# Performance work log

Measured on AMD Instinct MI355X. Metric: run time of the kernel, lower is better.

The kernel has to match this reference:

```python
import jax, jax.numpy as jnp
import numpy as np

N_WL = 296      # spectral points after dropping last 4
POOL = 4
FM = N_WL // POOL  # 74
HEAD = 64
EMB = 48


def setup_inputs() -> dict:
    key = jax.random.key(0)
    ks = jax.random.split(key, 16)
    B = 2048
    inp = {
        "x": jax.random.uniform(ks[0], (B, 300), dtype=jnp.float32),
        # FeaturePicker DI
        "wDI": jax.random.normal(ks[1], (HEAD, FM, FM), dtype=jnp.float32),
        "bDI": jax.random.normal(ks[2], (HEAD,), dtype=jnp.float32),
        "fcDI_w": jax.random.normal(ks[3], (EMB, HEAD), dtype=jnp.float32) * 0.1,
        "fcDI_b": jax.random.normal(ks[4], (EMB,), dtype=jnp.float32) * 0.1,
        # FeaturePicker NDI
        "wNDI": jax.random.normal(ks[5], (HEAD, FM, FM), dtype=jnp.float32),
        "bNDI": jax.random.normal(ks[6], (HEAD,), dtype=jnp.float32),
        "fcNDI_w": jax.random.normal(ks[7], (EMB, HEAD), dtype=jnp.float32) * 0.1,
        "fcNDI_b": jax.random.normal(ks[8], (EMB,), dtype=jnp.float32) * 0.1,
        # head MLP
        "fc1_w": jax.random.normal(ks[9], (48, 96), dtype=jnp.float32) * 0.1,
        "fc1_b": jax.random.normal(ks[10], (48,), dtype=jnp.float32) * 0.1,
        "l1_w": jax.random.normal(ks[11], (20, 48), dtype=jnp.float32) * 0.1,
        "l1_b": jax.random.normal(ks[12], (20,), dtype=jnp.float32) * 0.1,
        "l2_w": jax.random.normal(ks[13], (1, 20), dtype=jnp.float32) * 0.1,
        "l2_b": jax.random.normal(ks[14], (1,), dtype=jnp.float32) * 0.1,
    }
    return inp


def _feature_picker(m, wmap, bias, fw, fb):
    # m: [B, 296, 296] -> avgpool 4x4 -> [B, 74, 74]
    B = m.shape[0]
    p = m.reshape(B, FM, POOL, FM, POOL).mean(axis=(2, 4))
    # weighted sum against each of HEAD weight maps (== [B,5476] @ [5476,HEAD])
    h = jnp.einsum('bij,hij->bh', p, wmap) + bias
    h = jax.nn.elu(h)
    return jax.nn.elu(h @ fw.T + fb)  # [B, EMB]


def reference(x, wDI, bDI, fcDI_w, fcDI_b, wNDI, bNDI, fcNDI_w, fcNDI_b,
              fc1_w, fc1_b, l1_w, l1_b, l2_w, l2_b):
    x0 = x[:, :-4]                       # [B, 296]
    a = x0[:, None, :]                   # unsqueeze(1)
    b = x0[:, :, None]                   # unsqueeze(2)
    DI = a - b                           # [B, 296, 296]
    NDI = (a - b) / (a + b + 1e-5)
    eDI = _feature_picker(DI, wDI, bDI, fcDI_w, fcDI_b)
    eNDI = _feature_picker(NDI, wNDI, bNDI, fcNDI_w, fcNDI_b)
    emb = jnp.concatenate([eDI, eNDI], axis=1)      # [B, 96]
    emb = jax.nn.elu(emb @ fc1_w.T + fc1_b)
    emb = jax.nn.elu(emb @ l1_w.T + l1_b)
    return jax.nn.sigmoid(emb @ l2_w.T + l2_b)      # [B, 1]
```

## Files before the change

### kernel.cpp

```cpp
#include <hip/hip_runtime.h>
#include <hip/hip_bf16.h>
#include <math.h>

#define NWL    296
#define FMD    74
#define HEAD   64
#define EMBD   48
#define BATCH  2048
#define XCOLS  300
#define NPAIR  2701
#define NPAIR_P 3072
#define KCH    768
#define MR     8

#define WS_CMR  0
#define WS_PAIR (FMD * HEAD)
#define WS_WATT (WS_PAIR + NPAIR_P)

typedef _Float16 f16x8 __attribute__((ext_vector_type(8)));
typedef float f32x4 __attribute__((ext_vector_type(4)));

__device__ __forceinline__ float eluf(float x) { return x > 0.f ? x : expm1f(x); }

__device__ __forceinline__ void pair_decode(int k, int& I, int& J) {
  I = (int)((147.0f - sqrtf(21609.0f - 8.0f * (float)k)) * 0.5f);
  int base = (I * (147 - I)) >> 1;
  while (base > k) { I--; base = (I * (147 - I)) >> 1; }
  while (I < 72 && ((I + 1) * (146 - I)) / 2 <= k) { I++; base = (I * (147 - I)) >> 1; }
  J = I + 1 + (k - base);
}

__global__ __launch_bounds__(256) void fcr_prep_v5(
    const float* __restrict__ wDI,
    const float* __restrict__ wNDI,
    float* __restrict__ ws) {
  __shared__ float wdL[FMD * FMD];
  __shared__ float wnL[FMD * FMD];

  int t = threadIdx.x;
  int h = blockIdx.x;

  const float4* gd = (const float4*)(wDI + (size_t)h * FMD * FMD);
  const float4* gn = (const float4*)(wNDI + (size_t)h * FMD * FMD);
  for (int i = t; i < FMD * FMD / 4; i += 256) {
    ((float4*)wdL)[i] = gd[i];
    ((float4*)wnL)[i] = gn[i];
  }
  __syncthreads();

  _Float16* wATt = (_Float16*)(ws + WS_WATT);
  for (int k = t; k < NPAIR_P; k += 256) {
    float v = 0.f;
    if (k < NPAIR) {
      int I, J; pair_decode(k, I, J);
      v = (wnL[I * FMD + J] - wnL[J * FMD + I]) * 0.0625f;
    }
    wATt[(size_t)h * NPAIR_P + k] = (_Float16)v;
  }

  if (t < FMD) {
    int K = t;
    float cs = 0.f, rs = 0.f;
    for (int I = 0; I < FMD; I++) {
      cs += wdL[I * FMD + K];
      rs += wdL[K * FMD + I];
    }
    ws[WS_CMR + K * 64 + h] = cs - rs;
  }

  if (h == 0) {
    unsigned* P = (unsigned*)(ws + WS_PAIR);
    for (int k = t; k < NPAIR_P; k += 256) {
      unsigned pb = 0;
      if (k < NPAIR) {
        int I, J; pair_decode(k, I, J);
        pb = (unsigned)(4 * I) | ((unsigned)(4 * J) << 16);
      }
      P[k] = pb;
    }
  }
}

__global__ __launch_bounds__(256) void fcr_fused_v5(
    const float* __restrict__ x,
    const float* __restrict__ ws,
    const float* __restrict__ bDI,
    const float* __restrict__ fcDI_w,
    const float* __restrict__ fcDI_b,
    const float* __restrict__ bNDI,
    const float* __restrict__ fcNDI_w,
    const float* __restrict__ fcNDI_b,
    const float* __restrict__ fc1_w,
    const float* __restrict__ fc1_b,
    const float* __restrict__ l1_w,
    const float* __restrict__ l1_b,
    const float* __restrict__ l2_w,
    const float* __restrict__ l2_b,
    float* __restrict__ out) {
  __shared__ float xs[MR][308];
  __shared__ float xs4[MR][FMD];
  __shared__ _Float16 Sm[MR][776];
  __shared__ _Float16 wDT[HEAD * EMBD];
  __shared__ _Float16 wNT[HEAD * EMBD];
  __shared__ _Float16 w1T[96 * 48];
  __shared__ _Float16 wl1T[48 * 20];
  __shared__ float wl2s[20];
  __shared__ float bDs[HEAD], bNs[HEAD], bDe[EMBD], bNe[EMBD], b1[48], bl1s[20];
  __shared__ float bl2s;
  __shared__ float ehD[MR][68], ehN[MR][68];
  __shared__ float e2[MR][100];
  __shared__ float e3[MR][52];
  __shared__ float e4[MR][20];

  const unsigned* pairG = (const unsigned*)(ws + WS_PAIR);
  const _Float16* wATt = (const _Float16*)(ws + WS_WATT);
  const float* cmr = ws + WS_CMR;

  int t = threadIdx.x;
  int row0 = blockIdx.x * MR;

  for (int i = t; i < MR * (NWL / 4); i += 256) {
    int r = i / (NWL / 4), c4 = i - r * (NWL / 4);
    *(float4*)&xs[r][4 * c4] = *(const float4*)(x + (size_t)(row0 + r) * XCOLS + 4 * c4);
  }
  for (int i = t; i < HEAD * EMBD; i += 256) {
    int o = i >> 6, hh = i & 63;
    wDT[hh * EMBD + o] = (_Float16)fcDI_w[i];
    wNT[hh * EMBD + o] = (_Float16)fcNDI_w[i];
  }
  for (int i = t; i < 48 * 96; i += 256) {
    int o = i / 96, j = i - o * 96;
    w1T[j * 48 + o] = (_Float16)fc1_w[i];
  }
  for (int i = t; i < 20 * 48; i += 256) {
    int o = i / 48, j = i - o * 48;
    wl1T[j * 20 + o] = (_Float16)l1_w[i];
  }
  if (t < 20)   { wl2s[t] = l2_w[t]; bl1s[t] = l1_b[t]; }
  if (t < HEAD) { bDs[t] = bDI[t]; bNs[t] = bNDI[t]; }
  if (t < EMBD) { bDe[t] = fcDI_b[t]; bNe[t] = fcNDI_b[t]; }
  if (t < 48)   b1[t] = fc1_b[t];
  if (t == 0)   bl2s = l2_b[0];
  __syncthreads();

  for (int i = t; i < MR * FMD; i += 256) {
    int r = i / FMD, K = i - r * FMD;
    xs4[r][K] = 0.25f * (xs[r][4*K] + xs[r][4*K+1] + xs[r][4*K+2] + xs[r][4*K+3]);
  }
  __syncthreads();

  {
    int hh = t & 63, g = t >> 6;
    float d0 = 0.f, d1 = 0.f;
    for (int K = 0; K < FMD; K++) {
      float w = cmr[K * 64 + hh];
      d0 = fmaf(xs4[2*g][K],   w, d0);
      d1 = fmaf(xs4[2*g+1][K], w, d1);
    }
    ehD[2*g][hh]   = eluf(d0 + bDs[hh]);
    ehD[2*g+1][hh] = eluf(d1 + bDs[hh]);
  }

  int lane = t & 63;
  int wv   = t >> 6;
  int n_in = lane & 15;
  int quad = lane >> 4;
  int h    = wv * 16 + n_in;
  int mA   = t & 7;
  int kg   = t >> 3;

  f32x4 acc = {0.f, 0.f, 0.f, 0.f};

  for (int chunk = 0; chunk < NPAIR_P / KCH; chunk++) {
    int kbase = chunk * KCH;
    #pragma unroll 4
    for (int j = 0; j < KCH / 32; j++) {
      int kc = kg + 32 * j;
      unsigned pb = pairG[kbase + kc];
      int bI = pb & 0xFFFF, bJ = pb >> 16;
      float4 uv = *(const float4*)&xs[mA][bJ];
      float4 vv = *(const float4*)&xs[mA][bI];
      float u2[4] = { fmaf(2.f, uv.x, 1e-5f), fmaf(2.f, uv.y, 1e-5f),
                      fmaf(2.f, uv.z, 1e-5f), fmaf(2.f, uv.w, 1e-5f) };
      float u[4]  = { uv.x, uv.y, uv.z, uv.w };
      float v[4]  = { vv.x, vv.y, vv.z, vv.w };
      float s = 0.f;
      #pragma unroll
      for (int a = 0; a < 4; a++) {
        float va = v[a] + 1e-5f;
        #pragma unroll
        for (int b = 0; b < 4; b++)
          s = fmaf(u2[b], __builtin_amdgcn_rcpf(u[b] + va), s);
      }
      Sm[mA][kc] = (_Float16)(s - 16.f);
    }
    __syncthreads();

    #pragma unroll
    for (int c = 0; c < KCH / 32; c++) {
      f16x8 aF = *(const f16x8*)&Sm[n_in & 7][c * 32 + quad * 8];
      f16x8 bF = *(const f16x8*)&wATt[(size_t)h * NPAIR_P + kbase + c * 32 + quad * 8];
      acc = __builtin_amdgcn_mfma_f32_16x16x32_f16(aF, bF, acc, 0, 0, 0);
    }
    __syncthreads();
  }

  if (quad < 2) {
    #pragma unroll
    for (int r = 0; r < 4; r++) {
      int m = quad * 4 + r;
      ehN[m][h] = eluf(acc[r] + bNs[h]);
    }
  }
  __syncthreads();

  for (int i = t; i < MR * 96; i += 256) {
    int r = i / 96, o = i - r * 96;
    int isN = o >= 48;
    int o2 = isN ? o - 48 : o;
    const _Float16* wb = isN ? wNT : wDT;
    const float* eb = isN ? &ehN[r][0] : &ehD[r][0];
    float s = isN ? bNe[o2] : bDe[o2];
    for (int hh = 0; hh < 64; hh++)
      s = fmaf(eb[hh], (float)wb[hh * EMBD + o2], s);
    e2[r][o] = eluf(s);
  }
  __syncthreads();

  for (int i = t; i < MR * 48; i += 256) {
    int r = i / 48, o = i - r * 48;
    float s = b1[o];
    for (int j = 0; j < 96; j++)
      s = fmaf(e2[r][j], (float)w1T[j * 48 + o], s);
    e3[r][o] = eluf(s);
  }
  __syncthreads();

  if (t < MR * 20) {
    int r = t / 20, o = t - r * 20;
    float s = bl1s[o];
    for (int j = 0; j < 48; j++)
      s = fmaf(e3[r][j], (float)wl1T[j * 20 + o], s);
    e4[r][o] = eluf(s);
  }
  __syncthreads();

  if (t < MR) {
    float s = bl2s;
    for (int j = 0; j < 20; j++)
      s = fmaf(e4[t][j], wl2s[j], s);
    out[row0 + t] = 1.f / (1.f + expf(-s));
  }
}

extern "C" void kernel_launch(void* const* d_in, const int* in_sizes, int n_in,
                              void* d_out, int out_size, void* d_ws, size_t ws_size,
                              hipStream_t stream) {
  const float* x      = (const float*)d_in[0];
  const float* wDI    = (const float*)d_in[1];
  const float* bDI    = (const float*)d_in[2];
  const float* fcDI_w = (const float*)d_in[3];
  const float* fcDI_b = (const float*)d_in[4];
  const float* wNDI   = (const float*)d_in[5];
  const float* bNDI   = (const float*)d_in[6];
  const float* fcNDI_w= (const float*)d_in[7];
  const float* fcNDI_b= (const float*)d_in[8];
  const float* fc1_w  = (const float*)d_in[9];
  const float* fc1_b  = (const float*)d_in[10];
  const float* l1_w   = (const float*)d_in[11];
  const float* l1_b   = (const float*)d_in[12];
  const float* l2_w   = (const float*)d_in[13];
  const float* l2_b   = (const float*)d_in[14];
  float* out = (float*)d_out;
  float* ws = (float*)d_ws;

  fcr_prep_v5<<<HEAD, 256, 0, stream>>>(wDI, wNDI, ws);
  fcr_fused_v5<<<BATCH / MR, 256, 0, stream>>>(x, ws, bDI, fcDI_w, fcDI_b,
      bNDI, fcNDI_w, fcNDI_b, fc1_w, fc1_b, l1_w, l1_b, l2_w, l2_b, out);
}
```

Before: 137.1 us.

## Split NDI pair reduction across blocks and add a separate tail kernel

```diff
diff --git a/kernel.cpp b/kernel.cpp
--- a/kernel.cpp
+++ b/kernel.cpp
@@ -10,12 +10,14 @@
 #define XCOLS  300
 #define NPAIR  2701
 #define NPAIR_P 3072
-#define KCH    768
+#define KSPLIT 4
+#define SEGLEN (NPAIR_P / KSPLIT)
 #define MR     8
 
 #define WS_CMR  0
 #define WS_PAIR (FMD * HEAD)
 #define WS_WATT (WS_PAIR + NPAIR_P)
+#define WS_PNDI (WS_WATT + HEAD * NPAIR_P / 2)
 
 typedef _Float16 f16x8 __attribute__((ext_vector_type(8)));
 typedef float f32x4 __attribute__((ext_vector_type(4)));
@@ -30,7 +32,7 @@
   J = I + 1 + (k - base);
 }
 
-__global__ __launch_bounds__(256) void fcr_prep_v5(
+__global__ __launch_bounds__(256) void fcr_prep_v6(
     const float* __restrict__ wDI,
     const float* __restrict__ wNDI,
     float* __restrict__ ws) {
@@ -81,7 +83,77 @@
   }
 }
 
-__global__ __launch_bounds__(256) void fcr_fused_v5(
+__global__ __launch_bounds__(256, 4) void fcr_main_v6(
+    const float* __restrict__ x,
+    float* __restrict__ ws) {
+  __shared__ float xs[MR][308];
+  __shared__ _Float16 Sm[MR][776];
+  __shared__ unsigned pairsL[SEGLEN];
+
+  const unsigned* pairG = (const unsigned*)(ws + WS_PAIR);
+  const _Float16* wATt = (const _Float16*)(ws + WS_WATT);
+  float* pNDI = ws + WS_PNDI;
+
+  int t = threadIdx.x;
+  int seg = blockIdx.x & (KSPLIT - 1);
+  int row0 = (blockIdx.x >> 2) * MR;
+  int k0 = seg * SEGLEN;
+
+  for (int i = t; i < MR * (NWL / 4); i += 256) {
+    int r = i / (NWL / 4), c4 = i - r * (NWL / 4);
+    *(float4*)&xs[r][4 * c4] = *(const float4*)(x + (size_t)(row0 + r) * XCOLS + 4 * c4);
+  }
+  for (int i = t; i < SEGLEN; i += 256) pairsL[i] = pairG[k0 + i];
+  __syncthreads();
+
+  int mA = t & 7;
+  int kg = t >> 3;
+  #pragma unroll 4
+  for (int j = 0; j < SEGLEN / 32; j++) {
+    int kc = kg + 32 * j;
+    unsigned pb = pairsL[kc];
+    int bI = pb & 0xFFFF, bJ = pb >> 16;
+    float4 uv = *(const float4*)&xs[mA][bJ];
+    float4 vv = *(const float4*)&xs[mA][bI];
+    float u2[4] = { fmaf(2.f, uv.x, 1e-5f), fmaf(2.f, uv.y, 1e-5f),
+                    fmaf(2.f, uv.z, 1e-5f), fmaf(2.f, uv.w, 1e-5f) };
+    float u[4]  = { uv.x, uv.y, uv.z, uv.w };
+    float v[4]  = { vv.x, vv.y, vv.z, vv.w };
+    float s = 0.f;
+    #pragma unroll
+    for (int a = 0; a < 4; a++) {
+      float va = v[a] + 1e-5f;
+      #pragma unroll
+      for (int b = 0; b < 4; b++)
+        s = fmaf(u2[b], __builtin_amdgcn_rcpf(u[b] + va), s);
+    }
+    Sm[mA][kc] = (_Float16)(s - 16.f);
+  }
+  __syncthreads();
+
+  int lane = t & 63;
+  int wv   = t >> 6;
+  int n_in = lane & 15;
+  int quad = lane >> 4;
+  int h    = wv * 16 + n_in;
+  f32x4 acc = {0.f, 0.f, 0.f, 0.f};
+  #pragma unroll
+  for (int c = 0; c < SEGLEN / 32; c++) {
+    f16x8 aF = *(const f16x8*)&Sm[n_in & 7][c * 32 + quad * 8];
+    f16x8 bF = *(const f16x8*)&wATt[(size_t)h * NPAIR_P + k0 + c * 32 + quad * 8];
+    acc = __builtin_amdgcn_mfma_f32_16x16x32_f16(aF, bF, acc, 0, 0, 0);
+  }
+
+  if (quad < 2) {
+    #pragma unroll
+    for (int r = 0; r < 4; r++) {
+      int m = quad * 4 + r;
+      pNDI[((size_t)seg * BATCH + row0 + m) * 64 + h] = acc[r];
+    }
+  }
+}
+
+__global__ __launch_bounds__(256) void fcr_tail_v6(
     const float* __restrict__ x,
     const float* __restrict__ ws,
     const float* __restrict__ bDI,
@@ -99,7 +171,6 @@
     float* __restrict__ out) {
   __shared__ float xs[MR][308];
   __shared__ float xs4[MR][FMD];
-  __shared__ _Float16 Sm[MR][776];
   __shared__ _Float16 wDT[HEAD * EMBD];
   __shared__ _Float16 wNT[HEAD * EMBD];
   __shared__ _Float16 w1T[96 * 48];
@@ -112,9 +183,8 @@
   __shared__ float e3[MR][52];
   __shared__ float e4[MR][20];
 
-  const unsigned* pairG = (const unsigned*)(ws + WS_PAIR);
-  const _Float16* wATt = (const _Float16*)(ws + WS_WATT);
-  const float* cmr = ws + WS_CMR;
+  const float* cmr  = ws + WS_CMR;
+  const float* pNDI = ws + WS_PNDI;
 
   int t = threadIdx.x;
   int row0 = blockIdx.x * MR;
@@ -160,57 +230,13 @@
     ehD[2*g][hh]   = eluf(d0 + bDs[hh]);
     ehD[2*g+1][hh] = eluf(d1 + bDs[hh]);
   }
-
-  int lane = t & 63;
-  int wv   = t >> 6;
-  int n_in = lane & 15;
-  int quad = lane >> 4;
-  int h    = wv * 16 + n_in;
-  int mA   = t & 7;
-  int kg   = t >> 3;
-
-  f32x4 acc = {0.f, 0.f, 0.f, 0.f};
-
-  for (int chunk = 0; chunk < NPAIR_P / KCH; chunk++) {
-    int kbase = chunk * KCH;
-    #pragma unroll 4
-    for (int j = 0; j < KCH / 32; j++) {
-      int kc = kg + 32 * j;
-      unsigned pb = pairG[kbase + kc];
-      int bI = pb & 0xFFFF, bJ = pb >> 16;
-      float4 uv = *(const float4*)&xs[mA][bJ];
-      float4 vv = *(const float4*)&xs[mA][bI];
-      float u2[4] = { fmaf(2.f, uv.x, 1e-5f), fmaf(2.f, uv.y, 1e-5f),
-                      fmaf(2.f, uv.z, 1e-5f), fmaf(2.f, uv.w, 1e-5f) };
-      float u[4]  = { uv.x, uv.y, uv.z, uv.w };
-      float v[4]  = { vv.x, vv.y, vv.z, vv.w };
-      float s = 0.f;
-      #pragma unroll
-      for (int a = 0; a < 4; a++) {
-        float va = v[a] + 1e-5f;
-        #pragma unroll
-        for (int b = 0; b < 4; b++)
-          s = fmaf(u2[b], __builtin_amdgcn_rcpf(u[b] + va), s);
-      }
-      Sm[mA][kc] = (_Float16)(s - 16.f);
-    }
-    __syncthreads();
-
-    #pragma unroll
-    for (int c = 0; c < KCH / 32; c++) {
-      f16x8 aF = *(const f16x8*)&Sm[n_in & 7][c * 32 + quad * 8];
-      f16x8 bF = *(const f16x8*)&wATt[(size_t)h * NPAIR_P + kbase + c * 32 + quad * 8];
-      acc = __builtin_amdgcn_mfma_f32_16x16x32_f16(aF, bF, acc, 0, 0, 0);
-    }
-    __syncthreads();
-  }
-
-  if (quad < 2) {
-    #pragma unroll
-    for (int r = 0; r < 4; r++) {
-      int m = quad * 4 + r;
-      ehN[m][h] = eluf(acc[r] + bNs[h]);
-    }
+  for (int i = t; i < MR * HEAD; i += 256) {
+    int r = i >> 6, hh = i & 63;
+    int row = row0 + r;
+    float hN = bNs[hh];
+    for (int s2 = 0; s2 < KSPLIT; s2++)
+      hN += pNDI[((size_t)s2 * BATCH + row) * 64 + hh];
+    ehN[r][hh] = eluf(hN);
   }
   __syncthreads();
 
@@ -274,7 +300,8 @@
   float* out = (float*)d_out;
   float* ws = (float*)d_ws;
 
-  fcr_prep_v5<<<HEAD, 256, 0, stream>>>(wDI, wNDI, ws);
-  fcr_fused_v5<<<BATCH / MR, 256, 0, stream>>>(x, ws, bDI, fcDI_w, fcDI_b,
+  fcr_prep_v6<<<HEAD, 256, 0, stream>>>(wDI, wNDI, ws);
+  fcr_main_v6<<<(BATCH / MR) * KSPLIT, 256, 0, stream>>>(x, ws);
+  fcr_tail_v6<<<BATCH / MR, 256, 0, stream>>>(x, ws, bDI, fcDI_w, fcDI_b,
       bNDI, fcNDI_w, fcNDI_b, fc1_w, fc1_b, l1_w, l1_b, l2_w, l2_b, out);
 }
```

Result: faster. 127.3 us (-7.1%).
